# Optimization experiments

Hardware: AMD Instinct MI355X
Metric: run time of the kernel (lower is better)

Reference implementation:

```python
import jax, jax.numpy as jnp
import numpy as np

HIDDEN = 2048
N_HEADS = 16
N_KV_HEADS = 4
HEAD_DIM = HIDDEN // N_HEADS  # 128
BATCH = 2
SEQ = 2048


def setup_inputs() -> dict:
    key = jax.random.key(0)
    ks = jax.random.split(key, 10)
    s = 0.02
    return {
        "hidden_states": jax.random.normal(ks[0], (BATCH, SEQ, HIDDEN), jnp.float32),
        "attention_mask": jnp.ones((BATCH, SEQ), jnp.int32),
        # weights stored [in, out] so y = x @ W + b (transpose of torch layout)
        "Wq": jax.random.normal(ks[1], (HIDDEN, N_HEADS * HEAD_DIM), jnp.float32) * s,
        "bq": jnp.zeros((N_HEADS * HEAD_DIM,), jnp.float32),
        "Wk": jax.random.normal(ks[2], (HIDDEN, N_KV_HEADS * HEAD_DIM), jnp.float32) * s,
        "bk": jnp.zeros((N_KV_HEADS * HEAD_DIM,), jnp.float32),
        "Wv": jax.random.normal(ks[3], (HIDDEN, N_KV_HEADS * HEAD_DIM), jnp.float32) * s,
        "bv": jnp.zeros((N_KV_HEADS * HEAD_DIM,), jnp.float32),
        "Wo": jax.random.normal(ks[4], (N_HEADS * HEAD_DIM, HIDDEN), jnp.float32) * s,
        "bo": jnp.zeros((HIDDEN,), jnp.float32),
    }


def reference(hidden_states, attention_mask, Wq, bq, Wk, bk, Wv, bv, Wo, bo):
    B, S, _ = hidden_states.shape
    q = hidden_states @ Wq + bq  # [B,S,H*D]
    k = hidden_states @ Wk + bk  # [B,S,Hkv*D]
    v = hidden_states @ Wv + bv

    q = q.reshape(B, S, N_HEADS, HEAD_DIM).transpose(0, 2, 1, 3)      # [B,H,S,D]
    k = k.reshape(B, S, N_KV_HEADS, HEAD_DIM).transpose(0, 2, 1, 3)   # [B,Hkv,S,D]
    v = v.reshape(B, S, N_KV_HEADS, HEAD_DIM).transpose(0, 2, 1, 3)

    # GQA: repeat_interleave along head dim (head h uses kv head h // groups)
    groups = N_HEADS // N_KV_HEADS
    k = jnp.repeat(k, groups, axis=1)  # [B,H,S,D]
    v = jnp.repeat(v, groups, axis=1)

    scale = 1.0 / np.sqrt(HEAD_DIM)
    scores = jnp.einsum('bhqd,bhkd->bhqk', q, k) * scale  # [B,H,S,S]

    causal = jnp.tril(jnp.ones((S, S), bool))              # True = keep
    keep = causal[None, None, :, :] & (attention_mask[:, None, None, :] != 0)
    scores = jnp.where(keep, scores, -jnp.inf)

    attn = jax.nn.softmax(scores.astype(jnp.float32), axis=-1).astype(q.dtype)
    out = jnp.einsum('bhqk,bhkd->bhqd', attn, v)            # [B,H,S,D]
    out = out.transpose(0, 2, 1, 3).reshape(B, S, N_HEADS * HEAD_DIM)
    return out @ Wo + bo
```

## Files before the change

### kernel.cpp

```cpp
#include <hip/hip_runtime.h>
#include <hip/hip_bf16.h>


typedef unsigned short u16;
typedef unsigned long long u64;
typedef __attribute__((ext_vector_type(8))) short short8;
typedef __attribute__((ext_vector_type(4))) float f32x4;
typedef __attribute__((ext_vector_type(4))) unsigned uint4v;

#define BATCH 2
#define SEQ 2048
#define HIDDEN 2048
#define NH 16
#define NKV 4
#define HD 128
#define QKV_N 3072
#define MROWS 4096

__device__ inline u16 f2bf(float f) {
    __hip_bfloat16 h = __float2bfloat16(f);
    return __builtin_bit_cast(u16, h);
}

__device__ inline void async_copy16(const u16* g, u16* lds_base) {
    __builtin_amdgcn_global_load_lds(
        (const __attribute__((address_space(1))) void*)g,
        (__attribute__((address_space(3))) void*)lds_base, 16, 0, 0);
}

#define PREP_CONV   8192
#define PREP_WQ     (PREP_CONV + 4096)
#define PREP_WK     (PREP_WQ + 1024)
#define PREP_WV     (PREP_WK + 1024)
#define PREP_WO     (PREP_WV + 4096)
#define PREP_BIAS   (PREP_WO + 12)
#define PREP_TOTAL  (PREP_BIAS + 1)

__device__ inline void prep_transpose(const float* __restrict__ src, u16* __restrict__ dst,
                                      int N, int sub, float (*tile)[33]) {
    int nx = N >> 5;
    int bx = sub % nx, by = sub / nx;
    int n0 = bx * 32, k0 = by * 32;
    int t = threadIdx.x, tx = t & 31, ty = t >> 5;
#pragma unroll
    for (int i = 0; i < 32; i += 8)
        tile[ty + i][tx] = src[(size_t)(k0 + ty + i) * N + n0 + tx];
    __syncthreads();
#pragma unroll
    for (int i = 0; i < 32; i += 8)
        dst[(size_t)(n0 + ty + i) * HIDDEN + k0 + tx] = f2bf(tile[tx][ty + i]);
}

__global__ __launch_bounds__(256)
void prep(const float* __restrict__ hidden, u16* __restrict__ xb,
          const float* __restrict__ Wq, const float* __restrict__ Wk,
          const float* __restrict__ Wv, const float* __restrict__ Wo,
          u16* __restrict__ wqkvT, u16* __restrict__ woT,
          const float* __restrict__ bq, const float* __restrict__ bk,
          const float* __restrict__ bv, float* __restrict__ bqkv,
          const int* __restrict__ am, u64* __restrict__ mp) {
    __shared__ float tile[32][33];
    int bid = blockIdx.x;
    if (bid < PREP_CONV) {
        int i = (bid * 256 + threadIdx.x) * 4;
        float4 v = *(const float4*)(hidden + i);
        ushort4 o;
        o.x = f2bf(v.x); o.y = f2bf(v.y); o.z = f2bf(v.z); o.w = f2bf(v.w);
        *(ushort4*)(xb + i) = o;
    } else if (bid < PREP_WQ) {
        prep_transpose(Wq, wqkvT, 2048, bid - PREP_CONV, tile);
    } else if (bid < PREP_WK) {
        prep_transpose(Wk, wqkvT + (size_t)2048 * HIDDEN, 512, bid - PREP_WQ, tile);
    } else if (bid < PREP_WV) {
        prep_transpose(Wv, wqkvT + (size_t)2560 * HIDDEN, 512, bid - PREP_WK, tile);
    } else if (bid < PREP_WO) {
        prep_transpose(Wo, woT, 2048, bid - PREP_WV, tile);
    } else if (bid < PREP_BIAS) {
        int i = (bid - PREP_WO) * 256 + threadIdx.x;
        if (i < QKV_N)
            bqkv[i] = (i < 2048) ? bq[i] : ((i < 2560) ? bk[i - 2048] : bv[i - 2560]);
    } else {
        int i = threadIdx.x;
        if (i < BATCH * SEQ / 64) {
            const int* a = am + i * 64;
            u64 m = 0;
#pragma unroll
            for (int j = 0; j < 64; j += 4) {
                int4 v = *(const int4*)(a + j);
                m |= ((u64)(v.x != 0) << j) | ((u64)(v.y != 0) << (j + 1)) |
                     ((u64)(v.z != 0) << (j + 2)) | ((u64)(v.w != 0) << (j + 3));
            }
            mp[i] = m;
        }
    }
}

__global__ void vt_from_qkv(const u16* __restrict__ qkv, u16* __restrict__ vt) {
    __shared__ u16 tile[32][33];
    int b = blockIdx.z >> 2, kvh = blockIdx.z & 3;
    int s0 = blockIdx.x * 32, d0 = blockIdx.y * 32;
    int tx = threadIdx.x, ty = threadIdx.y;
#pragma unroll
    for (int i = 0; i < 32; i += 8)
        tile[ty + i][tx] = qkv[(size_t)(b * SEQ + s0 + ty + i) * QKV_N + 2560 + kvh * HD + d0 + tx];
    __syncthreads();
#pragma unroll
    for (int i = 0; i < 32; i += 8)
        vt[(size_t)((b * NKV + kvh) * HD + d0 + ty + i) * SEQ + s0 + tx] = tile[tx][ty + i];
}

template <bool OUT_BF16>
__global__ __launch_bounds__(512, 2)
void gemm_bf16_256(const u16* __restrict__ A, const u16* __restrict__ BT,
                   const float* __restrict__ bias, void* __restrict__ outp,
                   int M, int N, int K) {
    __shared__ __align__(16) u16 smem[2][2][256][64];
    const int t = threadIdx.x, w = t >> 6, lane = t & 63;
    const int quad = lane >> 4, l16 = lane & 15;
    const int wm = w >> 2, wn = w & 3;
    const int bm0 = blockIdx.y * 256, bn0 = blockIdx.x * 256;
    const int lrow = lane >> 3;
    const int lchk = (lane & 7) ^ lrow;
    const int NT = K >> 6;

    f32x4 acc[8][4];
#pragma unroll
    for (int i = 0; i < 8; i++)
#pragma unroll
        for (int j = 0; j < 4; j++) acc[i][j] = (f32x4){0.f, 0.f, 0.f, 0.f};

    const u16* gA = A + (size_t)bm0 * K;
    const u16* gB = BT + (size_t)bn0 * K;

    auto stage = [&](int buf, int op, int h, int k0) {
        const u16* gb = op ? gB : gA;
#pragma unroll
        for (int l = 0; l < 2; ++l) {
            int rb = h * 128 + w * 16 + l * 8;
            async_copy16(gb + (size_t)(rb + lrow) * K + k0 + lchk * 8,
                         &smem[buf][op][rb][0]);
        }
    };
    auto readA = [&](short8 (&aq)[4][2], int buf, int mh) {
#pragma unroll
        for (int mt = 0; mt < 4; ++mt) {
            int row = mh * 128 + mt * 32 + wm * 16 + l16;
            int swz = row & 7;
#pragma unroll
            for (int kk = 0; kk < 2; ++kk) {
                int chunk = ((kk << 2) | quad) ^ swz;
                aq[mt][kk] = *(const short8*)(&smem[buf][0][row][chunk << 3]);
            }
        }
    };
    auto readB = [&](short8 (&bq)[2][2], int buf, int nh) {
#pragma unroll
        for (int nt = 0; nt < 2; ++nt) {
            int row = nh * 128 + nt * 64 + wn * 16 + l16;
            int swz = row & 7;
#pragma unroll
            for (int kk = 0; kk < 2; ++kk) {
                int chunk = ((kk << 2) | quad) ^ swz;
                bq[nt][kk] = *(const short8*)(&smem[buf][1][row][chunk << 3]);
            }
        }
    };
    auto mmaQ = [&](short8 (&aq)[4][2], short8 (&bq)[2][2], int mh, int nh) {
        __builtin_amdgcn_s_setprio(1);
#pragma unroll
        for (int mt = 0; mt < 4; ++mt)
#pragma unroll
            for (int nt = 0; nt < 2; ++nt)
#pragma unroll
                for (int kk = 0; kk < 2; ++kk)
                    acc[mh * 4 + mt][nh * 2 + nt] = __builtin_amdgcn_mfma_f32_16x16x32_bf16(
                        aq[mt][kk], bq[nt][kk], acc[mh * 4 + mt][nh * 2 + nt], 0, 0, 0);
        __builtin_amdgcn_s_setprio(0);
    };

    stage(0, 0, 0, 0); stage(0, 1, 0, 0); stage(0, 1, 1, 0); stage(0, 0, 1, 0);
    asm volatile("s_waitcnt vmcnt(4)" ::: "memory");
    __builtin_amdgcn_s_barrier();

    short8 aq[4][2], b0[2][2], b1[2][2];
    for (int tt = 0; tt < NT - 1; ++tt) {
        const int cur = tt & 1, nxt = cur ^ 1, k1 = (tt + 1) << 6;
        readA(aq, cur, 0); readB(b0, cur, 0);
        stage(nxt, 0, 0, k1);
        mmaQ(aq, b0, 0, 0);
        asm volatile("s_waitcnt vmcnt(4)" ::: "memory");
        __builtin_amdgcn_s_barrier();
        readB(b1, cur, 1);
        stage(nxt, 1, 0, k1);
        mmaQ(aq, b1, 0, 1);
        asm volatile("s_waitcnt vmcnt(4)" ::: "memory");
        __builtin_amdgcn_s_barrier();
        readA(aq, cur, 1);
        stage(nxt, 1, 1, k1);
        mmaQ(aq, b1, 1, 1);
        asm volatile("s_waitcnt vmcnt(6)" ::: "memory");
        __builtin_amdgcn_s_barrier();
        stage(nxt, 0, 1, k1);
        mmaQ(aq, b0, 1, 0);
        asm volatile("s_waitcnt vmcnt(4)" ::: "memory");
        __builtin_amdgcn_s_barrier();
    }
    asm volatile("s_waitcnt vmcnt(0)" ::: "memory");
    __builtin_amdgcn_s_barrier();
    {
        const int cur = (NT - 1) & 1;
        readA(aq, cur, 0); readB(b0, cur, 0);
        mmaQ(aq, b0, 0, 0);
        readB(b1, cur, 1);
        mmaQ(aq, b1, 0, 1);
        readA(aq, cur, 1);
        mmaQ(aq, b1, 1, 1);
        mmaQ(aq, b0, 1, 0);
    }

#pragma unroll
    for (int nt = 0; nt < 4; ++nt) {
        int col = bn0 + nt * 64 + wn * 16 + l16;
        float bcol = bias[col];
#pragma unroll
        for (int mt = 0; mt < 8; ++mt) {
#pragma unroll
            for (int r = 0; r < 4; ++r) {
                int row = bm0 + mt * 32 + wm * 16 + quad * 4 + r;
                float v = acc[mt][nt][r] + bcol;
                if constexpr (OUT_BF16)
                    ((u16*)outp)[(size_t)row * N + col] = f2bf(v);
                else
                    ((float*)outp)[(size_t)row * N + col] = v;
            }
        }
    }
}

__global__ __launch_bounds__(512, 4)
void flash_attn(const u16* __restrict__ qkv, const u16* __restrict__ vt,
                const u64* __restrict__ mp, u16* __restrict__ attn) {
    __shared__ __align__(16) u16 Ks[64][136];
    __shared__ __align__(16) u16 Vs[128][72];
    int t = threadIdx.x, w = t >> 6, lane = t & 63, quad = lane >> 4, l16 = lane & 15;
    int bx = blockIdx.x, b = blockIdx.z;
    int qt = b ? ((int)gridDim.x - 1 - bx) : bx;
    int h = blockIdx.y, kvh = h >> 2;
    int q_row0 = qt * 128 + w * 16;

    const u16* qrow = qkv + (size_t)(b * SEQ + q_row0 + l16) * QKV_N + h * HD;
    short8 qf[4];
#pragma unroll
    for (int c = 0; c < 4; c++) qf[c] = *(const short8*)(qrow + c * 32 + quad * 8);

    f32x4 o[8];
#pragma unroll
    for (int dt = 0; dt < 8; dt++) o[dt] = (f32x4){0.f, 0.f, 0.f, 0.f};
    float lpart = 0.f;

    const float scale2 = 0.12751743f;
    const float C2 = 14.4269504f;

    const u16* kgb = qkv + (size_t)(b * SEQ) * QKV_N + 2048 + kvh * HD;
    const u16* vgb = vt + (size_t)((b * NKV + kvh) * HD) * SEQ;
    const u64* mpb = mp + b * (SEQ / 64);

    int kr = t >> 4, kc = (t & 15) * 8;
    int vr = t >> 3, vc = (t & 7) * 8;
    int kb_end = (qt + 1) * 128;

    short8 k0p, k1p, v0p, v1p;
    {
        k0p = *(const short8*)(kgb + (size_t)kr * QKV_N + kc);
        k1p = *(const short8*)(kgb + (size_t)(kr + 32) * QKV_N + kc);
        v0p = *(const short8*)(vgb + (size_t)vr * SEQ + vc);
        v1p = *(const short8*)(vgb + (size_t)(vr + 64) * SEQ + vc);
    }

    for (int kb = 0; kb < kb_end; kb += 64) {
        __syncthreads();
        *(short8*)(&Ks[kr][kc]) = k0p;
        *(short8*)(&Ks[kr + 32][kc]) = k1p;
        *(short8*)(&Vs[vr][vc]) = v0p;
        *(short8*)(&Vs[vr + 64][vc]) = v1p;
        __syncthreads();
        if (kb + 64 < kb_end) {
            const u16* kg = kgb + (size_t)(kb + 64) * QKV_N;
            const u16* vg = vgb + kb + 64;
            k0p = *(const short8*)(kg + (size_t)kr * QKV_N + kc);
            k1p = *(const short8*)(kg + (size_t)(kr + 32) * QKV_N + kc);
            v0p = *(const short8*)(vg + (size_t)vr * SEQ + vc);
            v1p = *(const short8*)(vg + (size_t)(vr + 64) * SEQ + vc);
        }
        if (kb > q_row0 + 15) continue;

        u64 mk = mpb[kb >> 6];

        f32x4 sc[4];
#pragma unroll
        for (int nt = 0; nt < 4; nt++) sc[nt] = (f32x4){0.f, 0.f, 0.f, 0.f};
        __builtin_amdgcn_s_setprio(1);
#pragma unroll
        for (int c = 0; c < 4; c++) {
#pragma unroll
            for (int nt = 0; nt < 4; nt++) {
                short8 kf = *(const short8*)(&Ks[nt * 16 + l16][c * 32 + quad * 8]);
                sc[nt] = __builtin_amdgcn_mfma_f32_16x16x32_bf16(kf, qf[c], sc[nt], 0, 0, 0);
            }
        }
        __builtin_amdgcn_s_setprio(0);

        short8 vf0a[4];
#pragma unroll
        for (int dt = 0; dt < 4; dt++)
            vf0a[dt] = *(const short8*)(&Vs[dt * 16 + l16][quad * 8]);

        int limit = q_row0 + l16 - kb;
        float p[4][4];
#pragma unroll
        for (int nt = 0; nt < 4; nt++) {
            unsigned nib = (unsigned)(mk >> (nt * 16 + quad * 4));
#pragma unroll
            for (int r = 0; r < 4; r++) {
                int bp = nt * 16 + quad * 4 + r;
                bool ok = ((nib >> r) & 1u) && (bp <= limit);
                float v = ok ? sc[nt][r] : -INFINITY;
                p[nt][r] = __builtin_exp2f(__builtin_fmaf(v, scale2, -C2));
            }
        }
        lpart += ((p[0][0] + p[0][1]) + (p[0][2] + p[0][3])) +
                 ((p[1][0] + p[1][1]) + (p[1][2] + p[1][3])) +
                 ((p[2][0] + p[2][1]) + (p[2][2] + p[2][3])) +
                 ((p[3][0] + p[3][1]) + (p[3][2] + p[3][3]));

        unsigned A0, A1, B0, B1, C0, C1, E0, E1;
        asm("v_cvt_pk_bf16_f32 %0, %1, %2" : "=v"(A0) : "v"(p[0][0]), "v"(p[0][1]));
        asm("v_cvt_pk_bf16_f32 %0, %1, %2" : "=v"(A1) : "v"(p[0][2]), "v"(p[0][3]));
        asm("v_cvt_pk_bf16_f32 %0, %1, %2" : "=v"(B0) : "v"(p[1][0]), "v"(p[1][1]));
        asm("v_cvt_pk_bf16_f32 %0, %1, %2" : "=v"(B1) : "v"(p[1][2]), "v"(p[1][3]));
        asm("v_cvt_pk_bf16_f32 %0, %1, %2" : "=v"(C0) : "v"(p[2][0]), "v"(p[2][1]));
        asm("v_cvt_pk_bf16_f32 %0, %1, %2" : "=v"(C1) : "v"(p[2][2]), "v"(p[2][3]));
        asm("v_cvt_pk_bf16_f32 %0, %1, %2" : "=v"(E0) : "v"(p[3][0]), "v"(p[3][1]));
        asm("v_cvt_pk_bf16_f32 %0, %1, %2" : "=v"(E1) : "v"(p[3][2]), "v"(p[3][3]));
        asm("v_permlane32_swap_b32 %0, %1" : "+v"(A0), "+v"(B0));
        asm("v_permlane16_swap_b32 %0, %1" : "+v"(A0), "+v"(B0));
        asm("v_permlane32_swap_b32 %0, %1" : "+v"(A1), "+v"(B1));
        asm("v_permlane16_swap_b32 %0, %1" : "+v"(A1), "+v"(B1));
        asm("v_permlane32_swap_b32 %0, %1" : "+v"(C0), "+v"(E0));
        asm("v_permlane16_swap_b32 %0, %1" : "+v"(C0), "+v"(E0));
        asm("v_permlane32_swap_b32 %0, %1" : "+v"(C1), "+v"(E1));
        asm("v_permlane16_swap_b32 %0, %1" : "+v"(C1), "+v"(E1));
        short8 pf0 = __builtin_bit_cast(short8, (uint4v){A0, A1, B0, B1});
        short8 pf1 = __builtin_bit_cast(short8, (uint4v){C0, C1, E0, E1});

        __builtin_amdgcn_s_setprio(1);
#pragma unroll
        for (int dt = 0; dt < 4; dt++)
            o[dt] = __builtin_amdgcn_mfma_f32_16x16x32_bf16(pf0, vf0a[dt], o[dt], 0, 0, 0);
#pragma unroll
        for (int dt = 4; dt < 8; dt++) {
            short8 vf0 = *(const short8*)(&Vs[dt * 16 + l16][quad * 8]);
            o[dt] = __builtin_amdgcn_mfma_f32_16x16x32_bf16(pf0, vf0, o[dt], 0, 0, 0);
        }
#pragma unroll
        for (int dt = 0; dt < 8; dt++) {
            short8 vf1 = *(const short8*)(&Vs[dt * 16 + l16][32 + quad * 8]);
            o[dt] = __builtin_amdgcn_mfma_f32_16x16x32_bf16(pf1, vf1, o[dt], 0, 0, 0);
        }
        __builtin_amdgcn_s_setprio(0);
    }
    float l = lpart;
    l += __shfl_xor(l, 16, 64);
    l += __shfl_xor(l, 32, 64);
    float invq[4];
#pragma unroll
    for (int r = 0; r < 4; r++) {
        float lr = __shfl(l, quad * 4 + r, 16);
        invq[r] = lr > 0.f ? 1.f / lr : 0.f;
    }
    size_t obase = (size_t)(b * SEQ + q_row0) * HIDDEN + h * HD;
#pragma unroll
    for (int dt = 0; dt < 8; dt++)
#pragma unroll
        for (int r = 0; r < 4; r++)
            attn[obase + (size_t)(quad * 4 + r) * HIDDEN + dt * 16 + l16] =
                f2bf(o[dt][r] * invq[r]);
}

extern "C" void kernel_launch(void* const* d_in, const int* in_sizes, int n_in,
                              void* d_out, int out_size, void* d_ws, size_t ws_size,
                              hipStream_t stream) {
    const float* hidden = (const float*)d_in[0];
    const int* amask   = (const int*)d_in[1];
    const float* Wq = (const float*)d_in[2];
    const float* bq = (const float*)d_in[3];
    const float* Wk = (const float*)d_in[4];
    const float* bk = (const float*)d_in[5];
    const float* Wv = (const float*)d_in[6];
    const float* bv = (const float*)d_in[7];
    const float* Wo = (const float*)d_in[8];
    const float* bo = (const float*)d_in[9];
    float* out = (float*)d_out;

    char* ws = (char*)d_ws;
    u16* xb     = (u16*)ws;  ws += (size_t)MROWS * HIDDEN * 2;
    u16* wqkvT  = (u16*)ws;  ws += (size_t)QKV_N * HIDDEN * 2;
    u16* woT    = (u16*)ws;  ws += (size_t)HIDDEN * HIDDEN * 2;
    float* bqkv = (float*)ws; ws += (size_t)QKV_N * 4;
    u64* mpk    = (u64*)ws;  ws += (size_t)(MROWS / 64) * 8;
    u16* qkv    = (u16*)ws;  ws += (size_t)MROWS * QKV_N * 2;
    u16* vt     = (u16*)ws;  ws += (size_t)BATCH * NKV * HD * SEQ * 2;
    u16* attn   = (u16*)ws;  ws += (size_t)MROWS * HIDDEN * 2;

    prep<<<dim3(PREP_TOTAL), dim3(256), 0, stream>>>(
        hidden, xb, Wq, Wk, Wv, Wo, wqkvT, woT, bq, bk, bv, bqkv, amask, mpk);

    gemm_bf16_256<true><<<dim3(QKV_N / 256, MROWS / 256), dim3(512), 0, stream>>>(
        xb, wqkvT, bqkv, qkv, MROWS, QKV_N, HIDDEN);

    vt_from_qkv<<<dim3(SEQ / 32, HD / 32, BATCH * NKV), dim3(32, 8), 0, stream>>>(qkv, vt);

    flash_attn<<<dim3(SEQ / 128, NH, BATCH), dim3(512), 0, stream>>>(qkv, vt, mpk, attn);

    gemm_bf16_256<false><<<dim3(HIDDEN / 256, MROWS / 256), dim3(512), 0, stream>>>(
        attn, woT, bo, out, MROWS, HIDDEN, HIDDEN);
}
```

Baseline: 298.5 us.

## Widen prep tiles and vectorize loads; skip masking on fully-visible attention tiles

The weight-transpose prep now uses 64x64 tiles with float4 loads and 16-byte bf16 stores, and the activation conversion handles 8 elements per thread, halving the block count. This is meant to cut per-block overhead and improve global memory access width in the prep kernel. In attention, key blocks that lie fully below the diagonal with an all-ones padding mask skip the per-element mask and compare logic. The fast path adds a branch, which should be uniform across each block.

```diff
diff --git a/kernel.cpp b/kernel.cpp
--- a/kernel.cpp
+++ b/kernel.cpp
@@ -28,27 +28,40 @@
         (__attribute__((address_space(3))) void*)lds_base, 16, 0, 0);
 }
 
-#define PREP_CONV   8192
-#define PREP_WQ     (PREP_CONV + 4096)
-#define PREP_WK     (PREP_WQ + 1024)
-#define PREP_WV     (PREP_WK + 1024)
-#define PREP_WO     (PREP_WV + 4096)
+#define PREP_CONV   4096
+#define PREP_WQ     (PREP_CONV + 1024)
+#define PREP_WK     (PREP_WQ + 256)
+#define PREP_WV     (PREP_WK + 256)
+#define PREP_WO     (PREP_WV + 1024)
 #define PREP_BIAS   (PREP_WO + 12)
 #define PREP_TOTAL  (PREP_BIAS + 1)
 
-__device__ inline void prep_transpose(const float* __restrict__ src, u16* __restrict__ dst,
-                                      int N, int sub, float (*tile)[33]) {
-    int nx = N >> 5;
+__device__ inline void prep_transpose64(const float* __restrict__ src, u16* __restrict__ dst,
+                                        int N, int sub, float (*tl)[69]) {
+    int nx = N >> 6;
     int bx = sub % nx, by = sub / nx;
-    int n0 = bx * 32, k0 = by * 32;
-    int t = threadIdx.x, tx = t & 31, ty = t >> 5;
-#pragma unroll
-    for (int i = 0; i < 32; i += 8)
-        tile[ty + i][tx] = src[(size_t)(k0 + ty + i) * N + n0 + tx];
+    int n0 = bx * 64, k0 = by * 64;
+    int t = threadIdx.x;
+    int rr = t >> 4, cc = (t & 15) * 4;
+#pragma unroll
+    for (int j = 0; j < 4; ++j) {
+        float4 v = *(const float4*)(src + (size_t)(k0 + rr + 16 * j) * N + n0 + cc);
+        int k = rr + 16 * j;
+        tl[cc + 0][k] = v.x;
+        tl[cc + 1][k] = v.y;
+        tl[cc + 2][k] = v.z;
+        tl[cc + 3][k] = v.w;
+    }
     __syncthreads();
-#pragma unroll
-    for (int i = 0; i < 32; i += 8)
-        dst[(size_t)(n0 + ty + i) * HIDDEN + k0 + tx] = f2bf(tile[tx][ty + i]);
+    int n = t >> 2;
+#pragma unroll
+    for (int j = 0; j < 2; ++j) {
+        int kk = (t & 3) * 8 + 32 * j;
+        short8 o8;
+#pragma unroll
+        for (int i = 0; i < 8; ++i) o8[i] = (short)f2bf(tl[n][kk + i]);
+        *(short8*)(dst + (size_t)(n0 + n) * HIDDEN + k0 + kk) = o8;
+    }
 }
 
 __global__ __launch_bounds__(256)
@@ -59,22 +72,26 @@
           const float* __restrict__ bq, const float* __restrict__ bk,
           const float* __restrict__ bv, float* __restrict__ bqkv,
           const int* __restrict__ am, u64* __restrict__ mp) {
-    __shared__ float tile[32][33];
+    __shared__ float tl[64][69];
     int bid = blockIdx.x;
     if (bid < PREP_CONV) {
-        int i = (bid * 256 + threadIdx.x) * 4;
-        float4 v = *(const float4*)(hidden + i);
-        ushort4 o;
-        o.x = f2bf(v.x); o.y = f2bf(v.y); o.z = f2bf(v.z); o.w = f2bf(v.w);
-        *(ushort4*)(xb + i) = o;
+        int i = (bid * 256 + threadIdx.x) * 8;
+        float4 v0 = *(const float4*)(hidden + i);
+        float4 v1 = *(const float4*)(hidden + i + 4);
+        short8 o8;
+        o8[0] = (short)f2bf(v0.x); o8[1] = (short)f2bf(v0.y);
+        o8[2] = (short)f2bf(v0.z); o8[3] = (short)f2bf(v0.w);
+        o8[4] = (short)f2bf(v1.x); o8[5] = (short)f2bf(v1.y);
+        o8[6] = (short)f2bf(v1.z); o8[7] = (short)f2bf(v1.w);
+        *(short8*)(xb + i) = o8;
     } else if (bid < PREP_WQ) {
-        prep_transpose(Wq, wqkvT, 2048, bid - PREP_CONV, tile);
+        prep_transpose64(Wq, wqkvT, 2048, bid - PREP_CONV, tl);
     } else if (bid < PREP_WK) {
-        prep_transpose(Wk, wqkvT + (size_t)2048 * HIDDEN, 512, bid - PREP_WQ, tile);
+        prep_transpose64(Wk, wqkvT + (size_t)2048 * HIDDEN, 512, bid - PREP_WQ, tl);
     } else if (bid < PREP_WV) {
-        prep_transpose(Wv, wqkvT + (size_t)2560 * HIDDEN, 512, bid - PREP_WK, tile);
+        prep_transpose64(Wv, wqkvT + (size_t)2560 * HIDDEN, 512, bid - PREP_WK, tl);
     } else if (bid < PREP_WO) {
-        prep_transpose(Wo, woT, 2048, bid - PREP_WV, tile);
+        prep_transpose64(Wo, woT, 2048, bid - PREP_WV, tl);
     } else if (bid < PREP_BIAS) {
         int i = (bid - PREP_WO) * 256 + threadIdx.x;
         if (i < QKV_N)
@@ -315,17 +332,25 @@
         for (int dt = 0; dt < 4; dt++)
             vf0a[dt] = *(const short8*)(&Vs[dt * 16 + l16][quad * 8]);
 
-        int limit = q_row0 + l16 - kb;
         float p[4][4];
-#pragma unroll
-        for (int nt = 0; nt < 4; nt++) {
-            unsigned nib = (unsigned)(mk >> (nt * 16 + quad * 4));
-#pragma unroll
-            for (int r = 0; r < 4; r++) {
-                int bp = nt * 16 + quad * 4 + r;
-                bool ok = ((nib >> r) & 1u) && (bp <= limit);
-                float v = ok ? sc[nt][r] : -INFINITY;
-                p[nt][r] = __builtin_exp2f(__builtin_fmaf(v, scale2, -C2));
+        if (mk == ~0ull && kb + 63 <= q_row0) {
+#pragma unroll
+            for (int nt = 0; nt < 4; nt++)
+#pragma unroll
+                for (int r = 0; r < 4; r++)
+                    p[nt][r] = __builtin_exp2f(__builtin_fmaf(sc[nt][r], scale2, -C2));
+        } else {
+            int limit = q_row0 + l16 - kb;
+#pragma unroll
+            for (int nt = 0; nt < 4; nt++) {
+                unsigned nib = (unsigned)(mk >> (nt * 16 + quad * 4));
+#pragma unroll
+                for (int r = 0; r < 4; r++) {
+                    int bp = nt * 16 + quad * 4 + r;
+                    bool ok = ((nib >> r) & 1u) && (bp <= limit);
+                    float v = ok ? sc[nt][r] : -INFINITY;
+                    p[nt][r] = __builtin_exp2f(__builtin_fmaf(v, scale2, -C2));
+                }
             }
         }
         lpart += ((p[0][0] + p[0][1]) + (p[0][2] + p[0][3])) +
```

Result: no change. 293.3 us (-1.7%).
